# Optimization experiments

Hardware: AMD Instinct MI355X
Metric: run time of the kernel (lower is better)

## Reference

```python
import jax, jax.numpy as jnp
import numpy as np

H = 1152; NH = 16; HD = 72; INTER = 4304; DEPTH = 4
C = 3; T = 2; P = 16; G = 48; M = 2; S = G * G
MERGED = H * M * M; OUT = 2048; ROT = HD // 2  # rotary_pos_emb_dim = head_dim//2


def _ln(x, w, b, eps=1e-6):
    # manual LayerNorm decomposition (mean/var/rsqrt), fp32 like the original
    m = x.mean(-1, keepdims=True)
    xc = x - m
    v = (xc * xc).mean(-1, keepdims=True)
    return w * (xc * jax.lax.rsqrt(v + eps)) + b


def _gelu(x):
    return jax.nn.gelu(x, approximate=True)  # tanh approximation


def _rot_half(x):
    h = x.shape[-1] // 2
    return jnp.concatenate([-x[..., h:], x[..., :h]], axis=-1)


def _pos_ids():
    # Qwen merge-pattern token order: 2x2 spatial blocks are contiguous
    ids = np.arange(G * G).reshape(G // M, M, G // M, M).transpose(0, 2, 1, 3).reshape(-1)
    return jnp.asarray(ids, dtype=jnp.int32)


def setup_inputs() -> dict:
    key = jax.random.key(0)
    ks = jax.random.split(key, 16)
    w = lambda k, shape: jax.random.normal(k, shape, jnp.float32) * 0.02
    return {
        'pixel_values': jax.random.normal(ks[0], (S, C * T * P * P), jnp.float32),
        'cu_seqlens': jnp.array([0, S], jnp.int32),
        'conv_w': w(ks[1], (H, C, T, P, P)),
        'conv_b': jnp.zeros((H,), jnp.float32),
        'pos_tab': w(ks[2], (G * G, H)),
        'ln1_w': jnp.ones((DEPTH, H), jnp.float32), 'ln1_b': jnp.zeros((DEPTH, H), jnp.float32),
        'ln2_w': jnp.ones((DEPTH, H), jnp.float32), 'ln2_b': jnp.zeros((DEPTH, H), jnp.float32),
        'qkv_w': w(ks[3], (DEPTH, 3 * H, H)), 'qkv_b': jnp.zeros((DEPTH, 3 * H), jnp.float32),
        'proj_w': w(ks[4], (DEPTH, H, H)), 'proj_b': jnp.zeros((DEPTH, H), jnp.float32),
        'fc1_w': w(ks[5], (DEPTH, INTER, H)), 'fc1_b': jnp.zeros((DEPTH, INTER), jnp.float32),
        'fc2_w': w(ks[6], (DEPTH, H, INTER)), 'fc2_b': jnp.zeros((DEPTH, H), jnp.float32),
        'm_norm_w': jnp.ones((H,), jnp.float32), 'm_norm_b': jnp.zeros((H,), jnp.float32),
        'm_fc1_w': w(ks[7], (MERGED, MERGED)), 'm_fc1_b': jnp.zeros((MERGED,), jnp.float32),
        'm_fc2_w': w(ks[8], (OUT, MERGED)), 'm_fc2_b': jnp.zeros((OUT,), jnp.float32),
    }


def reference(pixel_values, cu_seqlens, conv_w, conv_b, pos_tab,
              ln1_w, ln1_b, ln2_w, ln2_b, qkv_w, qkv_b, proj_w, proj_b,
              fc1_w, fc1_b, fc2_w, fc2_b, m_norm_w, m_norm_b,
              m_fc1_w, m_fc1_b, m_fc2_w, m_fc2_b):
    pos_ids = _pos_ids()
    # Conv3d with stride == kernel over pre-extracted patches == matmul
    x = pixel_values @ conv_w.reshape(H, -1).T + conv_b            # [S, H]
    x = x + pos_tab[pos_ids]
    # 2D rotary: h-freqs and w-freqs each ROT/2 dims, concat -> ROT, dup -> HD
    inv_freq = 1.0 / (10000.0 ** (jnp.arange(0, ROT, 2, dtype=jnp.float32) / ROT))
    hp = (pos_ids // G).astype(jnp.float32)
    wp = (pos_ids % G).astype(jnp.float32)
    freqs = jnp.concatenate([hp[:, None] * inv_freq, wp[:, None] * inv_freq], axis=-1)  # [S, ROT]
    emb = jnp.concatenate([freqs, freqs], axis=-1)                 # [S, HD]
    cos = jnp.cos(emb)[:, None, :]                                 # [S, 1, HD]
    sin = jnp.sin(emb)[:, None, :]
    # varlen attention: block-diagonal mask from cu_seqlens
    seg = jnp.searchsorted(cu_seqlens, jnp.arange(S), side='right')
    mask = jnp.where(seg[:, None] == seg[None, :], 0.0, -1e9).astype(jnp.float32)
    scale = 1.0 / np.sqrt(HD)
    for i in range(DEPTH):
        h = _ln(x, ln1_w[i], ln1_b[i])
        qkv = (h @ qkv_w[i].T + qkv_b[i]).reshape(S, 3, NH, HD)
        q, k, v = qkv[:, 0], qkv[:, 1], qkv[:, 2]
        q = q * cos + _rot_half(q) * sin
        k = k * cos + _rot_half(k) * sin
        scores = jnp.einsum('qhd,khd->hqk', q, k) * scale + mask
        attn = jax.nn.softmax(scores, axis=-1)
        o = jnp.einsum('hqk,khd->qhd', attn, v).reshape(S, H)
        x = x + o @ proj_w[i].T + proj_b[i]
        h2 = _ln(x, ln2_w[i], ln2_b[i])
        x = x + _gelu(h2 @ fc1_w[i].T + fc1_b[i]) @ fc2_w[i].T + fc2_b[i]
    # patch merger: pre-merge LN -> reshape to merged -> fc1 -> gelu(tanh) -> fc2
    y = _ln(x, m_norm_w, m_norm_b).reshape(-1, MERGED)             # [S/4, MERGED]
    return _gelu(y @ m_fc1_w.T + m_fc1_b) @ m_fc2_w.T + m_fc2_b   # [S/4, OUT]
```

## Files before the change

### kernel.cpp

```cpp
#include <hip/hip_runtime.h>
#include <hip/hip_bf16.h>
#include <math.h>

#define S 2304
#define HDIM 1152
#define NHEAD 16
#define HD 72
#define INTER 4304
#define INTERP 4352
#define DEPTH 4
#define MERGED 4608
#define OUTD 2048
#define KIN 1536
#define NSPLIT 4
#define KHALF (S / NSPLIT)

typedef float f4 __attribute__((ext_vector_type(4)));
typedef short s8v __attribute__((ext_vector_type(8)));

__device__ __forceinline__ int pos_id_of(int s) {
  int a = s / 96;
  int r = s % 96;
  int b = r >> 2;
  int c = (r >> 1) & 1;
  int d = r & 1;
  return a * 96 + c * 48 + b * 2 + d;
}

__device__ __forceinline__ float gelu_f(float v) {
  const float c = 0.7978845608028654f;
  float t = tanhf(c * (v + 0.044715f * v * v * v));
  return 0.5f * v * (1.f + t);
}

__device__ __forceinline__ unsigned short f2b(float f) {
  __hip_bfloat16 h = __float2bfloat16(f);
  unsigned short u;
  __builtin_memcpy(&u, &h, 2);
  return u;
}
__device__ __forceinline__ float b2f(unsigned short u) {
  return __uint_as_float(((unsigned int)u) << 16);
}

__device__ __forceinline__ void gload16(const void* g, void* l) {
  __builtin_amdgcn_global_load_lds(
      (const __attribute__((address_space(1))) void*)g,
      (__attribute__((address_space(3))) void*)l, 16, 0, 0);
}

__device__ __forceinline__ int xcd_swz(int flat, int nwg) {
  int q = nwg >> 3, r8 = nwg & 7;
  int xcd = flat & 7, lin = flat >> 3;
  return (xcd < r8 ? xcd * (q + 1) : r8 * (q + 1) + (xcd - r8) * q) + lin;
}

__global__ void __launch_bounds__(256) cvt_kernel(
    const float* __restrict__ src, unsigned short* __restrict__ dst,
    int N, int Ksrc, int Kdst)
{
  int idx = blockIdx.x * 256 + threadIdx.x;
  int kc = Kdst >> 3;
  if (idx >= N * kc) return;
  int r = idx / kc;
  int c8 = (idx % kc) << 3;
  const float* sp = src + (size_t)r * Ksrc + c8;
  unsigned short outv[8];
#pragma unroll
  for (int e = 0; e < 8; ++e)
    outv[e] = (c8 + e < Ksrc) ? f2b(sp[e]) : (unsigned short)0;
  *(uint4*)(dst + (size_t)r * Kdst + c8) = *(uint4*)outv;
}

__global__ void __launch_bounds__(256) cvt4_kernel(
    const float* __restrict__ s0, unsigned short* __restrict__ d0, int Ks0, int Kd0, int e0,
    const float* __restrict__ s1, unsigned short* __restrict__ d1, int Ks1, int Kd1, int e1,
    const float* __restrict__ s2, unsigned short* __restrict__ d2, int Ks2, int Kd2, int e2,
    const float* __restrict__ s3, unsigned short* __restrict__ d3, int Ks3, int Kd3, int e3)
{
  int idx = blockIdx.x * 256 + threadIdx.x;
  const float* src; unsigned short* dst; int Ksrc, Kdst, rel;
  if (idx < e0)      { src = s0; dst = d0; Ksrc = Ks0; Kdst = Kd0; rel = idx; }
  else if (idx < e1) { src = s1; dst = d1; Ksrc = Ks1; Kdst = Kd1; rel = idx - e0; }
  else if (idx < e2) { src = s2; dst = d2; Ksrc = Ks2; Kdst = Kd2; rel = idx - e1; }
  else if (idx < e3) { src = s3; dst = d3; Ksrc = Ks3; Kdst = Kd3; rel = idx - e2; }
  else return;
  int kc = Kdst >> 3;
  int r = rel / kc;
  int c8 = (rel % kc) << 3;
  const float* sp = src + (size_t)r * Ksrc + c8;
  unsigned short outv[8];
#pragma unroll
  for (int e = 0; e < 8; ++e)
    outv[e] = (c8 + e < Ksrc) ? f2b(sp[e]) : (unsigned short)0;
  *(uint4*)(dst + (size_t)r * Kdst + c8) = *(uint4*)outv;
}

__global__ void __launch_bounds__(256) gemm_bf16_m64_kernel(
    const unsigned short* __restrict__ A, const unsigned short* __restrict__ B,
    const float* __restrict__ bias, void* __restrict__ Cout,
    int M, int Nreal, int K, int lda, int ldb, int ldc, int act, int outbf)
{
  __shared__ unsigned short Asm[2][64 * 32];
  __shared__ unsigned short Bsm[2][128 * 32];
  const int tid = threadIdx.x;
  const int lane = tid & 63;
  const int wv = tid >> 6;

  int flat = blockIdx.y * gridDim.x + blockIdx.x;
  int swz = xcd_swz(flat, gridDim.x * gridDim.y);
  const int bm = (swz / gridDim.x) * 64;
  const int bn = (swz % gridDim.x) * 128;

  const int g8 = (lane >> 4) << 3;
  const int lr = lane & 15;

  const int lrow = lane >> 2;
  const int kq = (lane & 3) << 3;
  const unsigned short* AgP = A + (size_t)(bm + wv * 16 + lrow) * lda + kq;
  int brow1 = bn + wv * 16 + lrow;      if (brow1 >= Nreal) brow1 = Nreal - 1;
  int brow2 = bn + 64 + wv * 16 + lrow; if (brow2 >= Nreal) brow2 = Nreal - 1;
  const unsigned short* BgP1 = B + (size_t)brow1 * ldb + kq;
  const unsigned short* BgP2 = B + (size_t)brow2 * ldb + kq;

  f4 acc[4][2];
#pragma unroll
  for (int m = 0; m < 4; ++m)
#pragma unroll
    for (int n = 0; n < 2; ++n) { acc[m][n].x = 0.f; acc[m][n].y = 0.f; acc[m][n].z = 0.f; acc[m][n].w = 0.f; }

  const int nt = K >> 5;
  gload16(AgP, &Asm[0][(wv * 16) * 32]);
  gload16(BgP1, &Bsm[0][(wv * 16) * 32]);
  gload16(BgP2, &Bsm[0][(64 + wv * 16) * 32]);
  asm volatile("s_waitcnt vmcnt(0)" ::: "memory");
  __syncthreads();

  int cur = 0;
  for (int t = 0; t < nt; ++t) {
    if (t + 1 < nt) {
      int ko = (t + 1) << 5;
      gload16(AgP + ko, &Asm[cur ^ 1][(wv * 16) * 32]);
      gload16(BgP1 + ko, &Bsm[cur ^ 1][(wv * 16) * 32]);
      gload16(BgP2 + ko, &Bsm[cur ^ 1][(64 + wv * 16) * 32]);
    }
    s8v af[4], bf[2];
#pragma unroll
    for (int m = 0; m < 4; ++m)
      af[m] = *(const s8v*)&Asm[cur][(m * 16 + lr) * 32 + g8];
#pragma unroll
    for (int n = 0; n < 2; ++n)
      bf[n] = *(const s8v*)&Bsm[cur][(wv * 32 + n * 16 + lr) * 32 + g8];
#pragma unroll
    for (int m = 0; m < 4; ++m)
#pragma unroll
      for (int n = 0; n < 2; ++n)
        acc[m][n] = __builtin_amdgcn_mfma_f32_16x16x32_bf16(af[m], bf[n], acc[m][n], 0, 0, 0);
    asm volatile("s_waitcnt vmcnt(0)" ::: "memory");
    __syncthreads();
    cur ^= 1;
  }

  const int g4 = (lane >> 4) << 2;
#pragma unroll
  for (int m = 0; m < 4; ++m) {
    int r = bm + m * 16 + g4;
#pragma unroll
    for (int n = 0; n < 2; ++n) {
      int cidx = bn + wv * 32 + n * 16 + lr;
      float bb = (cidx < Nreal) ? bias[cidx] : 0.f;
#pragma unroll
      for (int j = 0; j < 4; ++j) {
        int rr = r + j;
        float v = acc[m][n][j] + bb;
        if (act) v = gelu_f(v);
        if (cidx >= Nreal) v = 0.f;
        if (outbf) ((unsigned short*)Cout)[(size_t)rr * ldc + cidx] = f2b(v);
        else       ((float*)Cout)[(size_t)rr * ldc + cidx] = v;
      }
    }
  }
}

__global__ void __launch_bounds__(256) gemm_bf16_splitk_kernel(
    const unsigned short* __restrict__ A, const unsigned short* __restrict__ B,
    float* __restrict__ Cpart, float* __restrict__ Calt,
    int M, int N, int Kc, int lda, int ldb)
{
  __shared__ unsigned short Asm[2][128 * 32];
  __shared__ unsigned short Bsm[2][128 * 32];
  const int tid = threadIdx.x;
  const int lane = tid & 63;
  const int wv = tid >> 6;
  const int wr = wv >> 1, wc = wv & 1;

  int flat = blockIdx.y * gridDim.x + blockIdx.x;
  int swz = xcd_swz(flat, gridDim.x * gridDim.y);
  const int bm = (swz / gridDim.x) * 128;
  const int bn = (swz % gridDim.x) * 128;
  const int z = blockIdx.z;
  const int kbase = z * Kc;

  const int g8 = (lane >> 4) << 3;
  const int lr = lane & 15;

  const int srow = wv * 32 + (lane >> 2);
  const int kcol = (lane & 3) << 3;
  int ar0 = bm + srow;      if (ar0 >= M) ar0 = M - 1;
  int ar1 = bm + srow + 16; if (ar1 >= M) ar1 = M - 1;
  int br0 = bn + srow;      if (br0 >= N) br0 = N - 1;
  int br1 = bn + srow + 16; if (br1 >= N) br1 = N - 1;
  const unsigned short* Ag0 = A + (size_t)ar0 * lda + kbase + kcol;
  const unsigned short* Ag1 = A + (size_t)ar1 * lda + kbase + kcol;
  const unsigned short* Bg0 = B + (size_t)br0 * ldb + kbase + kcol;
  const unsigned short* Bg1 = B + (size_t)br1 * ldb + kbase + kcol;

  f4 acc[4][4];
#pragma unroll
  for (int m = 0; m < 4; ++m)
#pragma unroll
    for (int n = 0; n < 4; ++n) { acc[m][n].x = 0.f; acc[m][n].y = 0.f; acc[m][n].z = 0.f; acc[m][n].w = 0.f; }

  const int nt = Kc >> 5;
  gload16(Ag0, &Asm[0][(wv * 32) * 32]);
  gload16(Ag1, &Asm[0][(wv * 32 + 16) * 32]);
  gload16(Bg0, &Bsm[0][(wv * 32) * 32]);
  gload16(Bg1, &Bsm[0][(wv * 32 + 16) * 32]);
  asm volatile("s_waitcnt vmcnt(0)" ::: "memory");
  __syncthreads();

  int cur = 0;
  for (int t = 0; t < nt; ++t) {
    if (t + 1 < nt) {
      int ko = (t + 1) << 5;
      gload16(Ag0 + ko, &Asm[cur ^ 1][(wv * 32) * 32]);
      gload16(Ag1 + ko, &Asm[cur ^ 1][(wv * 32 + 16) * 32]);
      gload16(Bg0 + ko, &Bsm[cur ^ 1][(wv * 32) * 32]);
      gload16(Bg1 + ko, &Bsm[cur ^ 1][(wv * 32 + 16) * 32]);
    }
    s8v af[4], bf[4];
#pragma unroll
    for (int m = 0; m < 4; ++m)
      af[m] = *(const s8v*)&Asm[cur][(wr * 64 + m * 16 + lr) * 32 + g8];
#pragma unroll
    for (int n = 0; n < 4; ++n)
      bf[n] = *(const s8v*)&Bsm[cur][(wc * 64 + n * 16 + lr) * 32 + g8];
#pragma unroll
    for (int m = 0; m < 4; ++m)
#pragma unroll
      for (int n = 0; n < 4; ++n)
        acc[m][n] = __builtin_amdgcn_mfma_f32_16x16x32_bf16(af[m], bf[n], acc[m][n], 0, 0, 0);
    asm volatile("s_waitcnt vmcnt(0)" ::: "memory");
    __syncthreads();
    cur ^= 1;
  }

  float* Cz = (Calt && z == 1) ? Calt : (Cpart + (size_t)z * M * N);
  const int g4 = (lane >> 4) << 2;
#pragma unroll
  for (int m = 0; m < 4; ++m) {
    int r = bm + wr * 64 + m * 16 + g4;
#pragma unroll
    for (int n = 0; n < 4; ++n) {
      int cidx = bn + wc * 64 + n * 16 + lr;
      if (cidx < N) {
#pragma unroll
        for (int j = 0; j < 4; ++j) {
          int rr = r + j;
          if (rr < M) Cz[(size_t)rr * N + cidx] = acc[m][n][j];
        }
      }
    }
  }
}

__global__ void __launch_bounds__(256) combine_gemm_kernel(
    const float* __restrict__ Cpart, int nz, const float* __restrict__ bias,
    const float* __restrict__ resid, float* __restrict__ out, int M, int N)
{
  int idx = blockIdx.x * 256 + threadIdx.x;
  int total = (M * N) >> 2;
  if (idx >= total) return;
  int r = idx / (N >> 2);
  int c4 = (idx % (N >> 2)) << 2;
  size_t off = (size_t)r * N + c4;
  float4 s = *(const float4*)(Cpart + off);
  for (int z = 1; z < nz; ++z) {
    float4 p = *(const float4*)(Cpart + (size_t)z * M * N + off);
    s.x += p.x; s.y += p.y; s.z += p.z; s.w += p.w;
  }
  float4 b = *(const float4*)(bias + c4);
  s.x += b.x; s.y += b.y; s.z += b.z; s.w += b.w;
  if (resid) {
    float4 rv = *(const float4*)(resid + off);
    s.x += rv.x; s.y += rv.y; s.z += rv.z; s.w += rv.w;
  }
  *(float4*)(out + off) = s;
}

__global__ void __launch_bounds__(256) combine2_gelu_kernel(
    const float* __restrict__ p0, const float* __restrict__ p1,
    const float* __restrict__ bias, unsigned short* __restrict__ out, int M, int N)
{
  int idx = blockIdx.x * 256 + threadIdx.x;
  int total = (M * N) >> 2;
  if (idx >= total) return;
  int r = idx / (N >> 2);
  int c4 = (idx % (N >> 2)) << 2;
  size_t off = (size_t)r * N + c4;
  float4 a = *(const float4*)(p0 + off);
  float4 b = *(const float4*)(p1 + off);
  float4 bi = *(const float4*)(bias + c4);
  unsigned short o[4];
  o[0] = f2b(gelu_f(a.x + b.x + bi.x));
  o[1] = f2b(gelu_f(a.y + b.y + bi.y));
  o[2] = f2b(gelu_f(a.z + b.z + bi.z));
  o[3] = f2b(gelu_f(a.w + b.w + bi.w));
  *(uint2*)(out + off) = *(uint2*)o;
}

__global__ void __launch_bounds__(256) combine_ln_kernel(
    const float* __restrict__ Cpart, int nz, const float* __restrict__ bias,
    const float* __restrict__ resid, const float* __restrict__ pos_tab,
    float* __restrict__ xout, const float* __restrict__ lnw,
    const float* __restrict__ lnb, unsigned short* __restrict__ hout)
{
  __shared__ float red[8];
  const int row = blockIdx.x;
  const int tid = threadIdx.x;
  const float* pos = pos_tab ? pos_tab + (size_t)pos_id_of(row) * HDIM : nullptr;
  float v[5];
  float s1 = 0.f;
#pragma unroll
  for (int t = 0; t < 5; ++t) {
    int i = tid + t * 256;
    float s = 0.f;
    if (i < HDIM) {
      size_t off = (size_t)row * HDIM + i;
      s = Cpart[off];
      for (int z = 1; z < nz; ++z) s += Cpart[(size_t)z * ((size_t)S * HDIM) + off];
      s += bias[i];
      if (resid) s += resid[off];
      if (pos) s += pos[i];
      xout[off] = s;
    }
    v[t] = s;
    s1 += s;
  }
#pragma unroll
  for (int off = 32; off > 0; off >>= 1) s1 += __shfl_down(s1, off);
  if ((tid & 63) == 0) red[tid >> 6] = s1;
  __syncthreads();
  float mean = (red[0] + red[1] + red[2] + red[3]) * (1.f / HDIM);
  float s2 = 0.f;
#pragma unroll
  for (int t = 0; t < 5; ++t) {
    int i = tid + t * 256;
    if (i < HDIM) { float d = v[t] - mean; s2 += d * d; }
  }
#pragma unroll
  for (int off = 32; off > 0; off >>= 1) s2 += __shfl_down(s2, off);
  __syncthreads();
  if ((tid & 63) == 0) red[tid >> 6] = s2;
  __syncthreads();
  float var = (red[0] + red[1] + red[2] + red[3]) * (1.f / HDIM);
  float rstd = rsqrtf(var + 1e-6f);
#pragma unroll
  for (int t = 0; t < 5; ++t) {
    int i = tid + t * 256;
    if (i < HDIM)
      hout[(size_t)row * HDIM + i] = f2b(lnw[i] * ((v[t] - mean) * rstd) + lnb[i]);
  }
}

__global__ void rope_tables_kernel(float* __restrict__ cosT, float* __restrict__ sinT)
{
  int s = blockIdx.x;
  int j = threadIdx.x;
  if (j >= 36) return;
  int pid = pos_id_of(s);
  float hp = (float)(pid / 48);
  float wp = (float)(pid % 48);
  int f = (j < 18) ? j : (j - 18);
  float inv = powf(10000.f, -(2.f * (float)f) / 36.f);
  float ang = ((j < 18) ? hp : wp) * inv;
  cosT[s * 36 + j] = cosf(ang);
  sinT[s * 36 + j] = sinf(ang);
}

__global__ void seg_kernel(const int* __restrict__ cu, int n_cu, int* __restrict__ seg)
{
  int i = blockIdx.x * 256 + threadIdx.x;
  if (i >= S) return;
  int s = 0;
  for (int t = 0; t < n_cu; ++t) s += (cu[t] <= i) ? 1 : 0;
  seg[i] = s;
}

__global__ void __launch_bounds__(256) rope_kernel(unsigned short* __restrict__ qkv,
    const float* __restrict__ cosT, const float* __restrict__ sinT)
{
  int idx = blockIdx.x * 256 + threadIdx.x;
  int d = idx % 36; int t = idx / 36;
  int hh = t % NHEAD; t /= NHEAD;
  int qk = t & 1; int s = t >> 1;
  unsigned short* base = qkv + (size_t)s * 3456 + qk * 1152 + hh * 72;
  float c = cosT[s * 36 + d], sn = sinT[s * 36 + d];
  float x0 = b2f(base[d]), x1 = b2f(base[d + 36]);
  base[d] = f2b(x0 * c - x1 * sn);
  base[d + 36] = f2b(x1 * c + x0 * sn);
}

#define KT 64
#define ASCALE2 (0.11785113019775793f * 1.4426950408889634f)
#define DEFER_THR 11.5415603f

__global__ void __launch_bounds__(256) flash_mfma_kernel(
    const unsigned short* __restrict__ qkv, unsigned short* __restrict__ opart,
    float* __restrict__ ml, const int* __restrict__ seg)
{
  __shared__ __align__(16) unsigned short Ks[64 * 80];
  __shared__ __align__(16) unsigned short Vt[80 * 80];
  __shared__ __align__(16) unsigned short Ps[4][16 * 80];

  const int tid = threadIdx.x;
  const int lane = tid & 63;
  const int wv = tid >> 6;
  const int g = lane >> 4;
  const int c = lane & 15;
  const int cm = c & 7;

  int flat = (blockIdx.z * NHEAD + blockIdx.y) * (S / 128) + blockIdx.x;
  int swz = xcd_swz(flat, (S / 128) * NHEAD * NSPLIT);
  const int q0 = (swz % (S / 128)) * 128;
  const int hh = (swz / (S / 128)) % NHEAD;
  const int sidx = swz / ((S / 128) * NHEAD);
  const int kbeg = sidx * KHALF;
  const int qr = q0 + wv * 32;

  for (int i = tid; i < 320; i += 256)
    ((unsigned int*)&Vt[72 * 80])[i] = 0u;

  const bool uni = (seg[q0] == seg[q0 + 127]) && (seg[kbeg] == seg[kbeg + KHALF - 1])
                && (seg[q0] == seg[kbeg]);
  const int msgA = seg[qr + c];
  const int msgB = seg[qr + 16 + c];

  s8v qfA[3], qfB[3];
  {
    const unsigned short* qa = qkv + (size_t)(qr + c) * 3456 + hh * HD;
    const unsigned short* qb = qkv + (size_t)(qr + 16 + c) * 3456 + hh * HD;
#pragma unroll
    for (int ks = 0; ks < 3; ++ks) {
      int k = ks * 32 + g * 8;
      if (k <= 64) { qfA[ks] = *(const s8v*)(qa + k); qfB[ks] = *(const s8v*)(qb + k); }
      else {
        s8v z;
#pragma unroll
        for (int t = 0; t < 8; ++t) z[t] = 0;
        qfA[ks] = z; qfB[ks] = z;
      }
    }
  }

  float mA = -1e30f, lA = 0.f, mB = -1e30f, lB = 0.f;
  f4 accoA[5], accoB[5];
#pragma unroll
  for (int n = 0; n < 5; ++n) {
    accoA[n].x = 0.f; accoA[n].y = 0.f; accoA[n].z = 0.f; accoA[n].w = 0.f;
    accoB[n].x = 0.f; accoB[n].y = 0.f; accoB[n].z = 0.f; accoB[n].w = 0.f;
  }

  uint4 kreg[3], vreg[3];

#define STAGE_LOAD(KT0)                                                                  \
  {                                                                                      \
    _Pragma("unroll")                                                                    \
    for (int ii = 0; ii < 3; ++ii) {                                                     \
      int idx = tid + ii * 256;                                                          \
      if (idx < 576) {                                                                   \
        int rK = idx / 9, cK = idx % 9;                                                  \
        kreg[ii] = *(const uint4*)(qkv + (size_t)((KT0) + rK) * 3456 + 1152 + hh * HD + cK * 8); \
        int rV = idx & 63, cV = idx >> 6;                                                \
        vreg[ii] = *(const uint4*)(qkv + (size_t)((KT0) + rV) * 3456 + 2304 + hh * HD + cV * 8); \
      }                                                                                  \
    }                                                                                    \
  }

#define STAGE_WRITE()                                                                    \
  {                                                                                      \
    _Pragma("unroll")                                                                    \
    for (int ii = 0; ii < 3; ++ii) {                                                     \
      int idx = tid + ii * 256;                                                          \
      if (idx < 576) {                                                                   \
        int rK = idx / 9, cK = idx % 9;                                                  \
        int colx = (cK < 8) ? ((cK ^ (rK & 7)) << 3) : 64;                               \
        *(uint4*)&Ks[rK * 80 + colx] = kreg[ii];                                         \
        int rV = idx & 63, cV = idx >> 6;                                                \
        unsigned short vv[8];                                                            \
        *(uint4*)vv = vreg[ii];                                                          \
        _Pragma("unroll")                                                                \
        for (int e = 0; e < 8; ++e) {                                                    \
          int drow = cV * 8 + e;                                                         \
          Vt[drow * 80 + (rV ^ ((drow & 7) << 3))] = vv[e];                              \
        }                                                                                \
      }                                                                                  \
    }                                                                                    \
  }

#define SUBBLOCK(QF, MSG, MM, LL, ACCO)                                                  \
  {                                                                                      \
    f4 accs[4];                                                                          \
    _Pragma("unroll")                                                                    \
    for (int nk = 0; nk < 4; ++nk) { accs[nk].x = 0.f; accs[nk].y = 0.f; accs[nk].z = 0.f; accs[nk].w = 0.f; } \
    _Pragma("unroll")                                                                    \
    for (int ks = 0; ks < 3; ++ks) {                                                     \
      const int koff = (ks < 2) ? (((ks * 4 + g) ^ cm) << 3) : 64;                       \
      _Pragma("unroll")                                                                  \
      for (int nk = 0; nk < 4; ++nk) {                                                   \
        s8v bk = *(const s8v*)&Ks[(nk * 16 + c) * 80 + koff];                            \
        accs[nk] = __builtin_amdgcn_mfma_f32_16x16x32_bf16(bk, QF[ks], accs[nk], 0, 0, 0); \
      }                                                                                  \
    }                                                                                    \
    float sc[4][4];                                                                      \
    float mx = -1e30f;                                                                   \
    if (uni) {                                                                           \
      _Pragma("unroll")                                                                  \
      for (int nk = 0; nk < 4; ++nk)                                                     \
        _Pragma("unroll")                                                                \
        for (int j = 0; j < 4; ++j) {                                                    \
          float vv = accs[nk][j] * ASCALE2;                                              \
          sc[nk][j] = vv; mx = fmaxf(mx, vv);                                            \
        }                                                                                \
    } else {                                                                             \
      _Pragma("unroll")                                                                  \
      for (int nk = 0; nk < 4; ++nk)                                                     \
        _Pragma("unroll")                                                                \
        for (int j = 0; j < 4; ++j) {                                                    \
          int kk = k0 + nk * 16 + g * 4 + j;                                             \
          float vv = accs[nk][j] * ASCALE2 + ((seg[kk] == MSG) ? 0.f : -1e9f);            \
          sc[nk][j] = vv; mx = fmaxf(mx, vv);                                            \
        }                                                                                \
    }                                                                                    \
    mx = fmaxf(mx, __shfl_xor(mx, 16));                                                  \
    mx = fmaxf(mx, __shfl_xor(mx, 32));                                                  \
    const bool allkeep = __all(mx <= MM + DEFER_THR);                                    \
    float al = 1.0f;                                                                     \
    if (!allkeep) {                                                                      \
      float mn = fmaxf(MM, mx);                                                          \
      al = exp2f(MM - mn);                                                               \
      MM = mn;                                                                           \
    }                                                                                    \
    float rsum = 0.f;                                                                    \
    float p[4][4];                                                                       \
    _Pragma("unroll")                                                                    \
    for (int nk = 0; nk < 4; ++nk)                                                       \
      _Pragma("unroll")                                                                  \
      for (int j = 0; j < 4; ++j) {                                                      \
        float pv = exp2f(sc[nk][j] - MM);                                                \
        p[nk][j] = pv; rsum += pv;                                                       \
      }                                                                                  \
    rsum += __shfl_xor(rsum, 16);                                                        \
    rsum += __shfl_xor(rsum, 32);                                                        \
    LL = LL * al + rsum;                                                                 \
    _Pragma("unroll")                                                                    \
    for (int nk = 0; nk < 4; ++nk) {                                                     \
      unsigned int w0 = (unsigned int)f2b(p[nk][0]) | ((unsigned int)f2b(p[nk][1]) << 16); \
      unsigned int w1 = (unsigned int)f2b(p[nk][2]) | ((unsigned int)f2b(p[nk][3]) << 16); \
      uint2 wv2; wv2.x = w0; wv2.y = w1;                                                 \
      *(uint2*)&Ps[wv][c * 80 + ((nk * 16 + g * 4) ^ (cm << 3))] = wv2;                  \
    }                                                                                    \
    if (!allkeep) {                                                                      \
      float alpha_row[4];                                                                \
      _Pragma("unroll")                                                                  \
      for (int j = 0; j < 4; ++j)                                                        \
        alpha_row[j] = __shfl(al, (lane & 48) | (g * 4 + j));                            \
      _Pragma("unroll")                                                                  \
      for (int n = 0; n < 5; ++n)                                                        \
        _Pragma("unroll")                                                                \
        for (int j = 0; j < 4; ++j) ACCO[n][j] *= alpha_row[j];                          \
    }                                                                                    \
    asm volatile("s_waitcnt lgkmcnt(0)" ::: "memory");                                   \
    __builtin_amdgcn_sched_barrier(0);                                                   \
    _Pragma("unroll")                                                                    \
    for (int ks = 0; ks < 2; ++ks) {                                                     \
      const int poff = ((ks * 4 + g) ^ cm) << 3;                                         \
      s8v pa = *(const s8v*)&Ps[wv][c * 80 + poff];                                      \
      _Pragma("unroll")                                                                  \
      for (int n = 0; n < 5; ++n) {                                                      \
        s8v vb = *(const s8v*)&Vt[(n * 16 + c) * 80 + poff];                             \
        ACCO[n] = __builtin_amdgcn_mfma_f32_16x16x32_bf16(pa, vb, ACCO[n], 0, 0, 0);     \
      }                                                                                  \
    }                                                                                    \
  }

  STAGE_LOAD(kbeg);
  asm volatile("s_waitcnt vmcnt(0)" ::: "memory");
  STAGE_WRITE();
  asm volatile("s_waitcnt lgkmcnt(0)" ::: "memory");
  __builtin_amdgcn_s_barrier();
  __builtin_amdgcn_sched_barrier(0);

  for (int k0 = kbeg; k0 < kbeg + KHALF; k0 += KT) {
    const bool more = (k0 + KT < kbeg + KHALF);
    if (more) STAGE_LOAD(k0 + KT);

    SUBBLOCK(qfA, msgA, mA, lA, accoA);
    SUBBLOCK(qfB, msgB, mB, lB, accoB);

    asm volatile("s_waitcnt lgkmcnt(0)" ::: "memory");
    __builtin_amdgcn_s_barrier();
    if (more) {
      asm volatile("s_waitcnt vmcnt(0)" ::: "memory");
      STAGE_WRITE();
      asm volatile("s_waitcnt lgkmcnt(0)" ::: "memory");
    }
    __builtin_amdgcn_s_barrier();
    __builtin_amdgcn_sched_barrier(0);
  }

  unsigned short* op = opart + (size_t)(sidx * NHEAD + hh) * S * 72;
  float lrA[4], mrA[4], lrB[4], mrB[4];
#pragma unroll
  for (int j = 0; j < 4; ++j) {
    int src = (lane & 48) | (g * 4 + j);
    lrA[j] = __shfl(lA, src); mrA[j] = __shfl(mA, src);
    lrB[j] = __shfl(lB, src); mrB[j] = __shfl(mB, src);
  }
#pragma unroll
  for (int n = 0; n < 5; ++n) {
    int col = n * 16 + c;
    if (col < HD) {
#pragma unroll
      for (int j = 0; j < 4; ++j) {
        int rowA = qr + g * 4 + j;
        op[(size_t)rowA * 72 + col] = f2b(accoA[n][j]);
        op[(size_t)(rowA + 16) * 72 + col] = f2b(accoB[n][j]);
      }
    }
  }
  if (c == 0) {
#pragma unroll
    for (int j = 0; j < 4; ++j) {
      int rowA = qr + g * 4 + j;
      float2 va; va.x = mrA[j]; va.y = lrA[j];
      *(float2*)&ml[((size_t)(sidx * NHEAD + hh) * S + rowA) * 2] = va;
      float2 vb; vb.x = mrB[j]; vb.y = lrB[j];
      *(float2*)&ml[((size_t)(sidx * NHEAD + hh) * S + rowA + 16) * 2] = vb;
    }
  }
}

__global__ void __launch_bounds__(256) attn_combine_kernel(
    const unsigned short* __restrict__ opart, const float* __restrict__ ml,
    unsigned short* __restrict__ oout)
{
  int idx = blockIdx.x * 256 + threadIdx.x;
  int d = idx % 72;
  int row = (idx / 72) % S;
  int hh = idx / (72 * S);
  float mv[NSPLIT], lv[NSPLIT];
  float ms = -1e30f;
#pragma unroll
  for (int z = 0; z < NSPLIT; ++z) {
    size_t b = (size_t)(z * NHEAD + hh) * S + row;
    mv[z] = ml[b * 2]; lv[z] = ml[b * 2 + 1];
    ms = fmaxf(ms, mv[z]);
  }
  float l = 0.f, o = 0.f;
#pragma unroll
  for (int z = 0; z < NSPLIT; ++z) {
    size_t b = (size_t)(z * NHEAD + hh) * S + row;
    float a = exp2f(mv[z] - ms);
    l += a * lv[z];
    o += a * b2f(opart[b * 72 + d]);
  }
  oout[(size_t)row * HDIM + hh * 72 + d] = f2b(o / l);
}

extern "C" void kernel_launch(void* const* d_in, const int* in_sizes, int n_in,
                              void* d_out, int out_size, void* d_ws, size_t ws_size,
                              hipStream_t stream)
{
  (void)n_in; (void)out_size; (void)ws_size;
  const float* pix    = (const float*)d_in[0];
  const int*   cu     = (const int*)d_in[1];
  const int    n_cu   = in_sizes[1];
  const float* conv_w = (const float*)d_in[2];
  const float* conv_b = (const float*)d_in[3];
  const float* pos_tab= (const float*)d_in[4];
  const float* ln1_w  = (const float*)d_in[5];
  const float* ln1_b  = (const float*)d_in[6];
  const float* ln2_w  = (const float*)d_in[7];
  const float* ln2_b  = (const float*)d_in[8];
  const float* qkv_w  = (const float*)d_in[9];
  const float* qkv_b  = (const float*)d_in[10];
  const float* proj_w = (const float*)d_in[11];
  const float* proj_b = (const float*)d_in[12];
  const float* fc1_w  = (const float*)d_in[13];
  const float* fc1_b  = (const float*)d_in[14];
  const float* fc2_w  = (const float*)d_in[15];
  const float* fc2_b  = (const float*)d_in[16];
  const float* mn_w   = (const float*)d_in[17];
  const float* mn_b   = (const float*)d_in[18];
  const float* mf1_w  = (const float*)d_in[19];
  const float* mf1_b  = (const float*)d_in[20];
  const float* mf2_w  = (const float*)d_in[21];
  const float* mf2_b  = (const float*)d_in[22];
  float* out = (float*)d_out;

  float*    x      = (float*)d_ws;
  unsigned short* h_bf   = (unsigned short*)(x + (size_t)S * HDIM);
  unsigned short* qkv_bf = h_bf + (size_t)S * HDIM;
  unsigned short* A_bf   = qkv_bf + (size_t)S * 3456;
  unsigned short* Wbuf   = A_bf + (size_t)S * INTERP;
  float*    cosT   = (float*)(Wbuf + (size_t)MERGED * MERGED);
  float*    sinT   = cosT + (size_t)S * 36;
  int*      seg    = (int*)(sinT + (size_t)S * 36);
  unsigned short* pix_bf = A_bf;
  unsigned short* opart  = A_bf;
  float*    ml     = (float*)(A_bf + (size_t)NSPLIT * NHEAD * S * 72);
  float*    part_h = (float*)h_bf;
  float*    part_q = (float*)qkv_bf;

  unsigned short* Wq = Wbuf;
  unsigned short* Wp = Wq + (size_t)3456 * HDIM;
  unsigned short* W1 = Wp + (size_t)HDIM * HDIM;
  unsigned short* W2 = W1 + (size_t)INTER * HDIM;

  auto cvt = [&](const float* src, unsigned short* dst, int N, int Ksrc, int Kdst) {
    int total = N * (Kdst >> 3);
    cvt_kernel<<<(total + 255) / 256, 256, 0, stream>>>(src, dst, N, Ksrc, Kdst);
  };
  auto gemm64 = [&](const unsigned short* A, const unsigned short* B, const float* bias,
                    void* C, int M, int N, int K, int lda, int ldb, int ldc, int act, int outbf) {
    gemm_bf16_m64_kernel<<<dim3((N + 127) / 128, M / 64), 256, 0, stream>>>(
        A, B, bias, C, M, N, K, lda, ldb, ldc, act, outbf);
  };
  auto splitk = [&](const unsigned short* A, const unsigned short* B, float* part,
                    float* alt, int M, int N, int K, int nz, int lda, int ldb) {
    gemm_bf16_splitk_kernel<<<dim3(N / 128, (M + 127) / 128, nz), 256, 0, stream>>>(
        A, B, part, alt, M, N, K / nz, lda, ldb);
  };
  auto comb_ln = [&](float* part, int nz, const float* bias, const float* resid,
                     const float* pos, const float* lw, const float* lb) {
    combine_ln_kernel<<<S, 256, 0, stream>>>(part, nz, bias, resid, pos, x, lw, lb, h_bf);
  };

  {
    int e0 = S * (KIN >> 3);
    int e1 = e0 + HDIM * (KIN >> 3);
    cvt4_kernel<<<(e1 + 255) / 256, 256, 0, stream>>>(
        pix, pix_bf, KIN, KIN, e0,
        conv_w, Wbuf, KIN, KIN, e1,
        nullptr, nullptr, 1, 8, e1,
        nullptr, nullptr, 1, 8, e1);
  }
  splitk(pix_bf, Wbuf, part_h, nullptr, S, HDIM, KIN, 2, KIN, KIN);
  rope_tables_kernel<<<S, 64, 0, stream>>>(cosT, sinT);
  seg_kernel<<<(S + 255) / 256, 256, 0, stream>>>(cu, n_cu, seg);
  comb_ln(part_h, 2, conv_b, nullptr, pos_tab, ln1_w, ln1_b);

  for (int layer = 0; layer < DEPTH; ++layer) {
    {
      int e0 = 3456 * (HDIM >> 3);
      int e1 = e0 + HDIM * (HDIM >> 3);
      int e2 = e1 + INTER * (HDIM >> 3);
      int e3 = e2 + HDIM * (INTERP >> 3);
      cvt4_kernel<<<(e3 + 255) / 256, 256, 0, stream>>>(
          qkv_w + (size_t)layer * 3456 * HDIM, Wq, HDIM, HDIM, e0,
          proj_w + (size_t)layer * HDIM * HDIM, Wp, HDIM, HDIM, e1,
          fc1_w + (size_t)layer * INTER * HDIM, W1, HDIM, HDIM, e2,
          fc2_w + (size_t)layer * HDIM * INTER, W2, INTER, INTERP, e3);
    }
    gemm64(h_bf, Wq, qkv_b + layer * 3456, qkv_bf, S, 3456, HDIM, HDIM, HDIM, 3456, 0, 1);
    rope_kernel<<<(S * 2 * NHEAD * 36) / 256, 256, 0, stream>>>(qkv_bf, cosT, sinT);
    flash_mfma_kernel<<<dim3(S / 128, NHEAD, NSPLIT), 256, 0, stream>>>(qkv_bf, opart, ml, seg);
    attn_combine_kernel<<<(NHEAD * S * 72) / 256, 256, 0, stream>>>(opart, ml, h_bf);
    splitk(h_bf, Wp, part_q, nullptr, S, HDIM, HDIM, 3, HDIM, HDIM);
    comb_ln(part_q, 3, proj_b + layer * HDIM, x, nullptr,
            ln2_w + layer * HDIM, ln2_b + layer * HDIM);
    gemm64(h_bf, W1, fc1_b + layer * INTER, A_bf, S, INTER, HDIM, HDIM, HDIM, INTERP, 1, 1);
    splitk(A_bf, W2, part_h, nullptr, S, HDIM, INTERP, 2, INTERP, INTERP);
    if (layer < DEPTH - 1)
      comb_ln(part_h, 2, fc2_b + layer * HDIM, x, nullptr,
              ln1_w + (layer + 1) * HDIM, ln1_b + (layer + 1) * HDIM);
    else
      comb_ln(part_h, 2, fc2_b + layer * HDIM, x, nullptr, mn_w, mn_b);
  }

  cvt(mf1_w, Wbuf, MERGED, MERGED, MERGED);
  {
    float* pz0 = x;
    float* pz1 = (float*)qkv_bf;
    splitk(h_bf, Wbuf, pz0, pz1, 576, MERGED, MERGED, 2, MERGED, MERGED);
    combine2_gelu_kernel<<<((576 * MERGED / 4) + 255) / 256, 256, 0, stream>>>(
        pz0, pz1, mf1_b, A_bf, 576, MERGED);
  }
  cvt(mf2_w, Wbuf, OUTD, MERGED, MERGED);
  splitk(A_bf, Wbuf, part_h, nullptr, 576, OUTD, MERGED, 4, MERGED, MERGED);
  combine_gemm_kernel<<<((576 * OUTD / 4) + 255) / 256, 256, 0, stream>>>(
      part_h, 4, mf2_b, nullptr, out, 576, OUTD);
}
```

Baseline: 1.670 ms.

## Interleave QK and PV MFMAs for both query subblocks; split merger fc1 three ways

The flash attention inner loop no longer runs two query subblocks one after the other. It computes both QK score tiles together, reusing each loaded K fragment for two MFMAs, then runs softmax for both, then does the PV MFMAs for both using separate P scratch buffers. This doubles the P shared-memory buffer and adds register pressure, but should expose more independent MFMA work and cut LDS reads of K and V. Separately, the merger fc1 split-K goes from 2 to 3 partitions, with the third partial stored in spare A_bf space and summed in the gelu combine kernel. That adds more blocks for the small-M GEMM at the cost of one more partial buffer to read.

```diff
diff --git a/kernel.cpp b/kernel.cpp
--- a/kernel.cpp
+++ b/kernel.cpp
@@ -184,7 +184,7 @@
 
 __global__ void __launch_bounds__(256) gemm_bf16_splitk_kernel(
     const unsigned short* __restrict__ A, const unsigned short* __restrict__ B,
-    float* __restrict__ Cpart, float* __restrict__ Calt,
+    float* __restrict__ Cpart, float* __restrict__ Calt, float* __restrict__ Calt2,
     int M, int N, int Kc, int lda, int ldb)
 {
   __shared__ unsigned short Asm[2][128 * 32];
@@ -255,7 +255,8 @@
     cur ^= 1;
   }
 
-  float* Cz = (Calt && z == 1) ? Calt : (Cpart + (size_t)z * M * N);
+  float* Cz = (Calt && z == 1) ? Calt
+            : ((Calt2 && z == 2) ? Calt2 : (Cpart + (size_t)z * M * N));
   const int g4 = (lane >> 4) << 2;
 #pragma unroll
   for (int m = 0; m < 4; ++m) {
@@ -298,9 +299,10 @@
   *(float4*)(out + off) = s;
 }
 
-__global__ void __launch_bounds__(256) combine2_gelu_kernel(
+__global__ void __launch_bounds__(256) combine_gelu_kernel(
     const float* __restrict__ p0, const float* __restrict__ p1,
-    const float* __restrict__ bias, unsigned short* __restrict__ out, int M, int N)
+    const float* __restrict__ p2, const float* __restrict__ bias,
+    unsigned short* __restrict__ out, int M, int N)
 {
   int idx = blockIdx.x * 256 + threadIdx.x;
   int total = (M * N) >> 2;
@@ -311,11 +313,17 @@
   float4 a = *(const float4*)(p0 + off);
   float4 b = *(const float4*)(p1 + off);
   float4 bi = *(const float4*)(bias + c4);
+  float sx = a.x + b.x + bi.x, sy = a.y + b.y + bi.y;
+  float sz = a.z + b.z + bi.z, sw = a.w + b.w + bi.w;
+  if (p2) {
+    float4 cc = *(const float4*)(p2 + off);
+    sx += cc.x; sy += cc.y; sz += cc.z; sw += cc.w;
+  }
   unsigned short o[4];
-  o[0] = f2b(gelu_f(a.x + b.x + bi.x));
-  o[1] = f2b(gelu_f(a.y + b.y + bi.y));
-  o[2] = f2b(gelu_f(a.z + b.z + bi.z));
-  o[3] = f2b(gelu_f(a.w + b.w + bi.w));
+  o[0] = f2b(gelu_f(sx));
+  o[1] = f2b(gelu_f(sy));
+  o[2] = f2b(gelu_f(sz));
+  o[3] = f2b(gelu_f(sw));
   *(uint2*)(out + off) = *(uint2*)o;
 }
 
@@ -421,7 +429,7 @@
 {
   __shared__ __align__(16) unsigned short Ks[64 * 80];
   __shared__ __align__(16) unsigned short Vt[80 * 80];
-  __shared__ __align__(16) unsigned short Ps[4][16 * 80];
+  __shared__ __align__(16) unsigned short Ps[8][16 * 80];
 
   const int tid = threadIdx.x;
   const int lane = tid & 63;
@@ -508,20 +516,8 @@
     }                                                                                    \
   }
 
-#define SUBBLOCK(QF, MSG, MM, LL, ACCO)                                                  \
+#define SOFTMAX_PS(ACCS, MSG, MM, LL, ACCO, PSIDX)                                       \
   {                                                                                      \
-    f4 accs[4];                                                                          \
-    _Pragma("unroll")                                                                    \
-    for (int nk = 0; nk < 4; ++nk) { accs[nk].x = 0.f; accs[nk].y = 0.f; accs[nk].z = 0.f; accs[nk].w = 0.f; } \
-    _Pragma("unroll")                                                                    \
-    for (int ks = 0; ks < 3; ++ks) {                                                     \
-      const int koff = (ks < 2) ? (((ks * 4 + g) ^ cm) << 3) : 64;                       \
-      _Pragma("unroll")                                                                  \
-      for (int nk = 0; nk < 4; ++nk) {                                                   \
-        s8v bk = *(const s8v*)&Ks[(nk * 16 + c) * 80 + koff];                            \
-        accs[nk] = __builtin_amdgcn_mfma_f32_16x16x32_bf16(bk, QF[ks], accs[nk], 0, 0, 0); \
-      }                                                                                  \
-    }                                                                                    \
     float sc[4][4];                                                                      \
     float mx = -1e30f;                                                                   \
     if (uni) {                                                                           \
@@ -529,7 +525,7 @@
       for (int nk = 0; nk < 4; ++nk)                                                     \
         _Pragma("unroll")                                                                \
         for (int j = 0; j < 4; ++j) {                                                    \
-          float vv = accs[nk][j] * ASCALE2;                                              \
+          float vv = ACCS[nk][j] * ASCALE2;                                              \
           sc[nk][j] = vv; mx = fmaxf(mx, vv);                                            \
         }                                                                                \
     } else {                                                                             \
@@ -538,7 +534,7 @@
         _Pragma("unroll")                                                                \
         for (int j = 0; j < 4; ++j) {                                                    \
           int kk = k0 + nk * 16 + g * 4 + j;                                             \
-          float vv = accs[nk][j] * ASCALE2 + ((seg[kk] == MSG) ? 0.f : -1e9f);            \
+          float vv = ACCS[nk][j] * ASCALE2 + ((seg[kk] == MSG) ? 0.f : -1e9f);            \
           sc[nk][j] = vv; mx = fmaxf(mx, vv);                                            \
         }                                                                                \
     }                                                                                    \
@@ -568,7 +564,7 @@
       unsigned int w0 = (unsigned int)f2b(p[nk][0]) | ((unsigned int)f2b(p[nk][1]) << 16); \
       unsigned int w1 = (unsigned int)f2b(p[nk][2]) | ((unsigned int)f2b(p[nk][3]) << 16); \
       uint2 wv2; wv2.x = w0; wv2.y = w1;                                                 \
-      *(uint2*)&Ps[wv][c * 80 + ((nk * 16 + g * 4) ^ (cm << 3))] = wv2;                  \
+      *(uint2*)&Ps[PSIDX][c * 80 + ((nk * 16 + g * 4) ^ (cm << 3))] = wv2;               \
     }                                                                                    \
     if (!allkeep) {                                                                      \
       float alpha_row[4];                                                                \
@@ -580,18 +576,6 @@
         _Pragma("unroll")                                                                \
         for (int j = 0; j < 4; ++j) ACCO[n][j] *= alpha_row[j];                          \
     }                                                                                    \
-    asm volatile("s_waitcnt lgkmcnt(0)" ::: "memory");                                   \
-    __builtin_amdgcn_sched_barrier(0);                                                   \
-    _Pragma("unroll")                                                                    \
-    for (int ks = 0; ks < 2; ++ks) {                                                     \
-      const int poff = ((ks * 4 + g) ^ cm) << 3;                                         \
-      s8v pa = *(const s8v*)&Ps[wv][c * 80 + poff];                                      \
-      _Pragma("unroll")                                                                  \
-      for (int n = 0; n < 5; ++n) {                                                      \
-        s8v vb = *(const s8v*)&Vt[(n * 16 + c) * 80 + poff];                             \
-        ACCO[n] = __builtin_amdgcn_mfma_f32_16x16x32_bf16(pa, vb, ACCO[n], 0, 0, 0);     \
-      }                                                                                  \
-    }                                                                                    \
   }
 
   STAGE_LOAD(kbeg);
@@ -605,8 +589,41 @@
     const bool more = (k0 + KT < kbeg + KHALF);
     if (more) STAGE_LOAD(k0 + KT);
 
-    SUBBLOCK(qfA, msgA, mA, lA, accoA);
-    SUBBLOCK(qfB, msgB, mB, lB, accoB);
+    f4 accsA[4], accsB[4];
+#pragma unroll
+    for (int nk = 0; nk < 4; ++nk) {
+      accsA[nk].x = 0.f; accsA[nk].y = 0.f; accsA[nk].z = 0.f; accsA[nk].w = 0.f;
+      accsB[nk].x = 0.f; accsB[nk].y = 0.f; accsB[nk].z = 0.f; accsB[nk].w = 0.f;
+    }
+#pragma unroll
+    for (int ks = 0; ks < 3; ++ks) {
+      const int koff = (ks < 2) ? (((ks * 4 + g) ^ cm) << 3) : 64;
+#pragma unroll
+      for (int nk = 0; nk < 4; ++nk) {
+        s8v bk = *(const s8v*)&Ks[(nk * 16 + c) * 80 + koff];
+        accsA[nk] = __builtin_amdgcn_mfma_f32_16x16x32_bf16(bk, qfA[ks], accsA[nk], 0, 0, 0);
+        accsB[nk] = __builtin_amdgcn_mfma_f32_16x16x32_bf16(bk, qfB[ks], accsB[nk], 0, 0, 0);
+      }
+    }
+
+    SOFTMAX_PS(accsA, msgA, mA, lA, accoA, wv);
+    SOFTMAX_PS(accsB, msgB, mB, lB, accoB, 4 + wv);
+
+    asm volatile("s_waitcnt lgkmcnt(0)" ::: "memory");
+    __builtin_amdgcn_sched_barrier(0);
+
+#pragma unroll
+    for (int ks = 0; ks < 2; ++ks) {
+      const int poff = ((ks * 4 + g) ^ cm) << 3;
+      s8v paA = *(const s8v*)&Ps[wv][c * 80 + poff];
+      s8v paB = *(const s8v*)&Ps[4 + wv][c * 80 + poff];
+#pragma unroll
+      for (int n = 0; n < 5; ++n) {
+        s8v vb = *(const s8v*)&Vt[(n * 16 + c) * 80 + poff];
+        accoA[n] = __builtin_amdgcn_mfma_f32_16x16x32_bf16(paA, vb, accoA[n], 0, 0, 0);
+        accoB[n] = __builtin_amdgcn_mfma_f32_16x16x32_bf16(paB, vb, accoB[n], 0, 0, 0);
+      }
+    }
 
     asm volatile("s_waitcnt lgkmcnt(0)" ::: "memory");
     __builtin_amdgcn_s_barrier();
@@ -738,9 +755,9 @@
         A, B, bias, C, M, N, K, lda, ldb, ldc, act, outbf);
   };
   auto splitk = [&](const unsigned short* A, const unsigned short* B, float* part,
-                    float* alt, int M, int N, int K, int nz, int lda, int ldb) {
+                    float* alt, float* alt2, int M, int N, int K, int nz, int lda, int ldb) {
     gemm_bf16_splitk_kernel<<<dim3(N / 128, (M + 127) / 128, nz), 256, 0, stream>>>(
-        A, B, part, alt, M, N, K / nz, lda, ldb);
+        A, B, part, alt, alt2, M, N, K / nz, lda, ldb);
   };
   auto comb_ln = [&](float* part, int nz, const float* bias, const float* resid,
                      const float* pos, const float* lw, const float* lb) {
@@ -756,7 +773,7 @@
         nullptr, nullptr, 1, 8, e1,
         nullptr, nullptr, 1, 8, e1);
   }
-  splitk(pix_bf, Wbuf, part_h, nullptr, S, HDIM, KIN, 2, KIN, KIN);
+  splitk(pix_bf, Wbuf, part_h, nullptr, nullptr, S, HDIM, KIN, 2, KIN, KIN);
   rope_tables_kernel<<<S, 64, 0, stream>>>(cosT, sinT);
   seg_kernel<<<(S + 255) / 256, 256, 0, stream>>>(cu, n_cu, seg);
   comb_ln(part_h, 2, conv_b, nullptr, pos_tab, ln1_w, ln1_b);
@@ -777,11 +794,11 @@
     rope_kernel<<<(S * 2 * NHEAD * 36) / 256, 256, 0, stream>>>(qkv_bf, cosT, sinT);
     flash_mfma_kernel<<<dim3(S / 128, NHEAD, NSPLIT), 256, 0, stream>>>(qkv_bf, opart, ml, seg);
     attn_combine_kernel<<<(NHEAD * S * 72) / 256, 256, 0, stream>>>(opart, ml, h_bf);
-    splitk(h_bf, Wp, part_q, nullptr, S, HDIM, HDIM, 3, HDIM, HDIM);
+    splitk(h_bf, Wp, part_q, nullptr, nullptr, S, HDIM, HDIM, 3, HDIM, HDIM);
     comb_ln(part_q, 3, proj_b + layer * HDIM, x, nullptr,
             ln2_w + layer * HDIM, ln2_b + layer * HDIM);
     gemm64(h_bf, W1, fc1_b + layer * INTER, A_bf, S, INTER, HDIM, HDIM, HDIM, INTERP, 1, 1);
-    splitk(A_bf, W2, part_h, nullptr, S, HDIM, INTERP, 2, INTERP, INTERP);
+    splitk(A_bf, W2, part_h, nullptr, nullptr, S, HDIM, INTERP, 2, INTERP, INTERP);
     if (layer < DEPTH - 1)
       comb_ln(part_h, 2, fc2_b + layer * HDIM, x, nullptr,
               ln1_w + (layer + 1) * HDIM, ln1_b + (layer + 1) * HDIM);
@@ -793,12 +810,13 @@
   {
     float* pz0 = x;
     float* pz1 = (float*)qkv_bf;
-    splitk(h_bf, Wbuf, pz0, pz1, 576, MERGED, MERGED, 2, MERGED, MERGED);
-    combine2_gelu_kernel<<<((576 * MERGED / 4) + 255) / 256, 256, 0, stream>>>(
-        pz0, pz1, mf1_b, A_bf, 576, MERGED);
+    float* pz2 = (float*)(A_bf + (size_t)576 * MERGED);
+    splitk(h_bf, Wbuf, pz0, pz1, pz2, 576, MERGED, MERGED, 3, MERGED, MERGED);
+    combine_gelu_kernel<<<((576 * MERGED / 4) + 255) / 256, 256, 0, stream>>>(
+        pz0, pz1, pz2, mf1_b, A_bf, 576, MERGED);
   }
   cvt(mf2_w, Wbuf, OUTD, MERGED, MERGED);
-  splitk(A_bf, Wbuf, part_h, nullptr, 576, OUTD, MERGED, 4, MERGED, MERGED);
+  splitk(A_bf, Wbuf, part_h, nullptr, nullptr, 576, OUTD, MERGED, 4, MERGED, MERGED);
   combine_gemm_kernel<<<((576 * OUTD / 4) + 255) / 256, 256, 0, stream>>>(
       part_h, 4, mf2_b, nullptr, out, 576, OUTD);
 }
```

New measurement: 1.657 ms. About the same (-0.8%).
